# Kernel optimization log

Hardware: AMD Instinct MI355X
Metric: run time of the kernel (lower is better)

Reference implementation:

```python
import jax, jax.numpy as jnp
import numpy as np

B, E = 256, 512
C, K = 8192, 10          # n_class, n_center
LMD = 10.0
INV_GAMMA = 10.0         # 1 / gamma, gamma = 0.1
TAU = 0.2
MARGIN = 0.01


def setup_inputs() -> dict:
    key = jax.random.key(0)
    k1, k2, k3 = jax.random.split(key, 3)
    embeddings = jax.random.normal(k1, (B, E), dtype=jnp.float32)
    labels = jax.random.randint(k2, (B,), 0, C, dtype=jnp.int64)
    fc = jax.random.normal(k3, (C * K, E), dtype=jnp.float32)
    return {"embeddings": embeddings, "labels": labels, "fc": fc}


def reference(embeddings, labels, fc):
    # L2-normalize centers (rows of fc), like F.normalize(fc, p=2, dim=1)
    norm = jnp.sqrt(jnp.sum(fc * fc, axis=1, keepdims=True))
    w = fc / jnp.maximum(norm, 1e-12)

    # similarity to every center: [B, C, K]
    x = (embeddings @ w.T).reshape(B, C, K)
    prob = jax.nn.softmax(INV_GAMMA * x, axis=2)
    h = jnp.sum(prob * x, axis=2)  # [B, C] soft-pooled class similarity

    # subtract margin on ground-truth class, then cross-entropy
    rows = jnp.arange(B)
    margin_m = jnp.zeros_like(h).at[rows, labels].set(MARGIN)
    logits = LMD * (h - margin_m)
    logp = jax.nn.log_softmax(logits, axis=1)
    loss_cls = -jnp.mean(logp[rows, labels])

    # regularizer: batched per-class center gram, replaces python loop over C
    wc = w.reshape(C, K, E)
    sub = 1.0 - jnp.einsum('cke,cje->ckj', wc, wc)   # [C, K, K]
    sub = jnp.where(sub <= 0.0, 1e-10, sub)
    mask = jnp.triu(jnp.ones((K, K), dtype=bool), k=1)  # strict upper triangle
    safe = jnp.where(mask, 2.0 * sub, 1.0)
    reg = jnp.sum(jnp.where(mask, jnp.sqrt(safe), 0.0))
    reg = reg / (C * K * (K - 1.0))
    return loss_cls + TAU * reg
```

## Files before the change

### kernel.cpp

```cpp
#include <hip/hip_runtime.h>


typedef __bf16 bf16;
typedef bf16 bf16x8 __attribute__((ext_vector_type(8)));
typedef float f32x4 __attribute__((ext_vector_type(4)));

#define NCLASS 8192
#define KC 10
#define KPAD 16
#define EDIM 512
#define BATCH 256

__device__ inline void load_lds16(const void* g, void* l) {
    __builtin_amdgcn_global_load_lds(
        (const __attribute__((address_space(1))) void*)g,
        (__attribute__((address_space(3))) void*)l, 16, 0, 0);
}

__global__ __launch_bounds__(256) void prep_kernel(
    const float* __restrict__ fc, bf16* __restrict__ wpad,
    float* __restrict__ gram_part)
{
    __shared__ float rows[KC * EDIM];
    __shared__ float s_invn[KC];
    __shared__ float s_wsum[4];
    const int c = blockIdx.x;
    const int t = threadIdx.x;
    const int wave = t >> 6, lane = t & 63;

    const float4* src = (const float4*)(fc + (size_t)c * (KC * EDIM));
    float4* rows4 = (float4*)rows;
    #pragma unroll
    for (int i = 0; i < 5; ++i) rows4[t + i * 256] = src[t + i * 256];
    __syncthreads();

    for (int r = wave; r < KC; r += 4) {
        float s = 0.f;
        #pragma unroll
        for (int j = 0; j < 8; ++j) {
            float v = rows[r * EDIM + lane + j * 64];
            s += v * v;
        }
        #pragma unroll
        for (int off = 32; off; off >>= 1) s += __shfl_xor(s, off);
        if (lane == 0) s_invn[r] = 1.0f / fmaxf(sqrtf(s), 1e-12f);
    }
    __syncthreads();

    bf16x8* dst = (bf16x8*)(wpad + (size_t)c * (KPAD * EDIM));
    #pragma unroll
    for (int p = 0; p < 4; ++p) {
        int j = t + p * 256;
        int r = j >> 6;
        bf16x8 v;
        if (r < KC) {
            float inv = s_invn[r];
            float4 a = *(const float4*)(rows + j * 8);
            float4 b = *(const float4*)(rows + j * 8 + 4);
            v[0] = (bf16)(a.x * inv); v[1] = (bf16)(a.y * inv);
            v[2] = (bf16)(a.z * inv); v[3] = (bf16)(a.w * inv);
            v[4] = (bf16)(b.x * inv); v[5] = (bf16)(b.y * inv);
            v[6] = (bf16)(b.z * inv); v[7] = (bf16)(b.w * inv);
        } else {
            #pragma unroll
            for (int u = 0; u < 8; ++u) v[u] = (bf16)0.0f;
        }
        dst[j] = v;
    }

    float part = 0.f;
    for (int p = wave; p < 45; p += 4) {
        int i = 0, pp = p;
        while (pp >= 9 - i) { pp -= 9 - i; ++i; }
        int j = i + 1 + pp;
        float s = 0.f;
        #pragma unroll
        for (int u = 0; u < 8; ++u)
            s += rows[i * EDIM + lane + u * 64] * rows[j * EDIM + lane + u * 64];
        #pragma unroll
        for (int off = 32; off; off >>= 1) s += __shfl_xor(s, off);
        if (lane == 0) {
            float sub = 1.0f - s * s_invn[i] * s_invn[j];
            if (sub <= 0.0f) sub = 1e-10f;
            part += sqrtf(2.0f * sub);
        }
    }
    if (lane == 0) s_wsum[wave] = part;
    __syncthreads();
    if (t == 0) gram_part[c] = s_wsum[0] + s_wsum[1] + s_wsum[2] + s_wsum[3];
}

__global__ __launch_bounds__(256) void conv_kernel(
    const float* __restrict__ e, bf16* __restrict__ out)
{
    int i = blockIdx.x * 256 + threadIdx.x;
    float4 a = ((const float4*)e)[i * 2];
    float4 b = ((const float4*)e)[i * 2 + 1];
    bf16x8 v;
    v[0] = (bf16)a.x; v[1] = (bf16)a.y; v[2] = (bf16)a.z; v[3] = (bf16)a.w;
    v[4] = (bf16)b.x; v[5] = (bf16)b.y; v[6] = (bf16)b.z; v[7] = (bf16)b.w;
    ((bf16x8*)out)[i] = v;
}

__global__ __launch_bounds__(512) void gemm_h_kernel(
    const bf16* __restrict__ W,
    const bf16* __restrict__ A,
    float* __restrict__ h)
{
    __shared__ bf16 Ws[128 * 32];
    __shared__ bf16 Es[256 * 32];
    const int tid = threadIdx.x;
    const int wave = tid >> 6, lane = tid & 63;
    const int wm = wave & 1, wn = wave >> 1;
    const size_t m0 = (size_t)blockIdx.x * 128;

    f32x4 acc[4][4];
    #pragma unroll
    for (int mt = 0; mt < 4; ++mt)
        #pragma unroll
        for (int nt = 0; nt < 4; ++nt)
            acc[mt][nt] = (f32x4){0.f, 0.f, 0.f, 0.f};

    const int lrow = lane >> 2;
    const int lcol = (lane & 3) * 8;

    for (int kb = 0; kb < EDIM; kb += 32) {
        load_lds16(W + (m0 + wave * 16 + lrow) * EDIM + kb + lcol,
                   Ws + (wave * 16) * 32);
        #pragma unroll
        for (int p = 0; p < 2; ++p) {
            int row = p * 128 + wave * 16 + lrow;
            load_lds16(A + row * EDIM + kb + lcol,
                       Es + (p * 128 + wave * 16) * 32);
        }
        __syncthreads();

        const int q8 = (lane >> 4) * 8;
        bf16x8 wf[4], ef[4];
        #pragma unroll
        for (int mt = 0; mt < 4; ++mt)
            wf[mt] = *(const bf16x8*)&Ws[(wm * 64 + mt * 16 + (lane & 15)) * 32 + q8];
        #pragma unroll
        for (int nt = 0; nt < 4; ++nt)
            ef[nt] = *(const bf16x8*)&Es[(wn * 64 + nt * 16 + (lane & 15)) * 32 + q8];
        #pragma unroll
        for (int mt = 0; mt < 4; ++mt)
            #pragma unroll
            for (int nt = 0; nt < 4; ++nt)
                acc[mt][nt] = __builtin_amdgcn_mfma_f32_16x16x32_bf16(
                    wf[mt], ef[nt], acc[mt][nt], 0, 0, 0);
        __syncthreads();
    }

    const int col = lane & 15;
    const int quad = lane >> 4;
    #pragma unroll
    for (int mt = 0; mt < 4; ++mt) {
        int cls = blockIdx.x * 8 + wm * 4 + mt;
        #pragma unroll
        for (int nt = 0; nt < 4; ++nt) {
            int b = wn * 64 + nt * 16 + col;
            float xm = -1e30f;
            #pragma unroll
            for (int r = 0; r < 4; ++r)
                if (quad * 4 + r < KC) xm = fmaxf(xm, acc[mt][nt][r]);
            xm = fmaxf(xm, __shfl_xor(xm, 16));
            xm = fmaxf(xm, __shfl_xor(xm, 32));
            float s1 = 0.f, s2 = 0.f;
            #pragma unroll
            for (int r = 0; r < 4; ++r) {
                if (quad * 4 + r < KC) {
                    float x = acc[mt][nt][r];
                    float e = __expf(10.0f * (x - xm));
                    s1 += e; s2 += e * x;
                }
            }
            s1 += __shfl_xor(s1, 16); s1 += __shfl_xor(s1, 32);
            s2 += __shfl_xor(s2, 16); s2 += __shfl_xor(s2, 32);
            if (quad == 0) h[(size_t)b * NCLASS + cls] = s2 / s1;
        }
    }
}

__global__ __launch_bounds__(256) void ce_kernel(
    const float* __restrict__ h, const int* __restrict__ labels,
    float* __restrict__ ce_part)
{
    __shared__ float redm[4];
    __shared__ float reds[4];
    const int b = blockIdx.x, t = threadIdx.x;
    const int wave = t >> 6, lane = t & 63;
    const int lbl = labels[b];
    const float* hb = h + (size_t)b * NCLASS;

    float lg_cache[32];
    float mx = -1e30f;
    #pragma unroll
    for (int k = 0; k < 32; ++k) {
        int c = t + k * 256;
        float lg = 10.0f * hb[c];
        if (c == lbl) lg -= 0.1f;
        lg_cache[k] = lg;
        mx = fmaxf(mx, lg);
    }
    #pragma unroll
    for (int off = 32; off; off >>= 1) mx = fmaxf(mx, __shfl_xor(mx, off));
    if (lane == 0) redm[wave] = mx;
    __syncthreads();
    mx = fmaxf(fmaxf(redm[0], redm[1]), fmaxf(redm[2], redm[3]));

    float s = 0.f;
    #pragma unroll
    for (int k = 0; k < 32; ++k) s += __expf(lg_cache[k] - mx);
    #pragma unroll
    for (int off = 32; off; off >>= 1) s += __shfl_xor(s, off);
    if (lane == 0) reds[wave] = s;
    __syncthreads();
    if (t == 0) {
        s = reds[0] + reds[1] + reds[2] + reds[3];
        float logit_l = 10.0f * (hb[lbl] - 0.01f);
        ce_part[b] = mx + logf(s) - logit_l;
    }
}

__global__ __launch_bounds__(256) void final_kernel(
    const float* __restrict__ gram_part, const float* __restrict__ ce_part,
    float* __restrict__ out)
{
    __shared__ float red[4];
    const int t = threadIdx.x, wave = t >> 6, lane = t & 63;
    float g = 0.f;
    #pragma unroll
    for (int i = 0; i < 32; ++i) g += gram_part[t + i * 256];
    float val = ce_part[t] * (1.0f / 256.0f)
              + g * (0.2f / 737280.0f);
    #pragma unroll
    for (int off = 32; off; off >>= 1) val += __shfl_xor(val, off);
    if (lane == 0) red[wave] = val;
    __syncthreads();
    if (t == 0) out[0] = red[0] + red[1] + red[2] + red[3];
}

extern "C" void kernel_launch(void* const* d_in, const int* in_sizes, int n_in,
                              void* d_out, int out_size, void* d_ws, size_t ws_size,
                              hipStream_t stream) {
    const float* emb    = (const float*)d_in[0];
    const int*   labels = (const int*)d_in[1];
    const float* fc     = (const float*)d_in[2];
    float* out = (float*)d_out;

    char* ws = (char*)d_ws;
    bf16*  wpad      = (bf16*)ws;
    bf16*  embb      = (bf16*)(ws + 134217728);
    float* h         = (float*)(ws + 134479872);
    float* gram_part = (float*)(ws + 142868480);
    float* ce_part   = (float*)(ws + 142901248);

    prep_kernel<<<NCLASS, 256, 0, stream>>>(fc, wpad, gram_part);
    conv_kernel<<<64, 256, 0, stream>>>(emb, embb);
    gemm_h_kernel<<<131072 / 128, 512, 0, stream>>>(wpad, embb, h);
    ce_kernel<<<BATCH, 256, 0, stream>>>(h, labels, ce_part);
    final_kernel<<<1, 256, 0, stream>>>(gram_part, ce_part, out);
}
```

Measured before the change: 326.6 us.

## Store unnormalized bf16 centers unpadded, apply norms in GEMM epilogue, split CE

The prep kernel now writes raw bf16 centers with no padding from 10 to 16 rows, plus a per-class inverse-norm table, and computes norms and the gram regularizer from the bf16 copy. The GEMM drops LDS staging and barriers, loads fragments straight from global memory, and scales by inverse norms before the soft-pool epilogue. h is written transposed, and cross-entropy becomes a class-split online softmax that a final kernel merges. This aims to cut weight write and read traffic and to spread the CE work over more blocks, at the cost of uncoalesced direct global fragment loads and computing the regularizer from bf16 values.

```diff
diff --git a/kernel.cpp b/kernel.cpp
--- a/kernel.cpp
+++ b/kernel.cpp
@@ -3,91 +3,83 @@
 
 typedef __bf16 bf16;
 typedef bf16 bf16x8 __attribute__((ext_vector_type(8)));
+typedef bf16 bf16x4 __attribute__((ext_vector_type(4)));
+typedef bf16 bf16x2 __attribute__((ext_vector_type(2)));
 typedef float f32x4 __attribute__((ext_vector_type(4)));
 
 #define NCLASS 8192
 #define KC 10
-#define KPAD 16
 #define EDIM 512
 #define BATCH 256
 
-__device__ inline void load_lds16(const void* g, void* l) {
-    __builtin_amdgcn_global_load_lds(
-        (const __attribute__((address_space(1))) void*)g,
-        (__attribute__((address_space(3))) void*)l, 16, 0, 0);
-}
-
-__global__ __launch_bounds__(256) void prep_kernel(
-    const float* __restrict__ fc, bf16* __restrict__ wpad,
-    float* __restrict__ gram_part)
-{
-    __shared__ float rows[KC * EDIM];
+__global__ __launch_bounds__(320) void prep_kernel(
+    const float* __restrict__ fc, bf16* __restrict__ w,
+    float* __restrict__ invn, float* __restrict__ gram_part)
+{
+    __shared__ bf16 rb[KC * EDIM];
     __shared__ float s_invn[KC];
-    __shared__ float s_wsum[4];
-    const int c = blockIdx.x;
-    const int t = threadIdx.x;
+    __shared__ float s_part[5];
+    const int c = blockIdx.x, t = threadIdx.x;
     const int wave = t >> 6, lane = t & 63;
 
     const float4* src = (const float4*)(fc + (size_t)c * (KC * EDIM));
-    float4* rows4 = (float4*)rows;
-    #pragma unroll
-    for (int i = 0; i < 5; ++i) rows4[t + i * 256] = src[t + i * 256];
-    __syncthreads();
-
-    for (int r = wave; r < KC; r += 4) {
+    bf16x4* wdst = (bf16x4*)(w + (size_t)c * (KC * EDIM));
+    bf16x4* ldst = (bf16x4*)rb;
+    #pragma unroll
+    for (int p = 0; p < 4; ++p) {
+        int idx = t + p * 320;
+        float4 v = src[idx];
+        bf16x4 bv;
+        bv[0] = (bf16)v.x; bv[1] = (bf16)v.y;
+        bv[2] = (bf16)v.z; bv[3] = (bf16)v.w;
+        ldst[idx] = bv;
+        wdst[idx] = bv;
+    }
+    __syncthreads();
+
+    #pragma unroll
+    for (int rr = 0; rr < 2; ++rr) {
+        int r = wave * 2 + rr;
         float s = 0.f;
         #pragma unroll
-        for (int j = 0; j < 8; ++j) {
-            float v = rows[r * EDIM + lane + j * 64];
-            s += v * v;
+        for (int j = 0; j < 4; ++j) {
+            bf16x2 v = *(const bf16x2*)&rb[r * EDIM + (lane + j * 64) * 2];
+            float a = (float)v[0], b = (float)v[1];
+            s += a * a + b * b;
         }
         #pragma unroll
         for (int off = 32; off; off >>= 1) s += __shfl_xor(s, off);
         if (lane == 0) s_invn[r] = 1.0f / fmaxf(sqrtf(s), 1e-12f);
     }
     __syncthreads();
-
-    bf16x8* dst = (bf16x8*)(wpad + (size_t)c * (KPAD * EDIM));
-    #pragma unroll
-    for (int p = 0; p < 4; ++p) {
-        int j = t + p * 256;
-        int r = j >> 6;
-        bf16x8 v;
-        if (r < KC) {
-            float inv = s_invn[r];
-            float4 a = *(const float4*)(rows + j * 8);
-            float4 b = *(const float4*)(rows + j * 8 + 4);
-            v[0] = (bf16)(a.x * inv); v[1] = (bf16)(a.y * inv);
-            v[2] = (bf16)(a.z * inv); v[3] = (bf16)(a.w * inv);
-            v[4] = (bf16)(b.x * inv); v[5] = (bf16)(b.y * inv);
-            v[6] = (bf16)(b.z * inv); v[7] = (bf16)(b.w * inv);
-        } else {
-            #pragma unroll
-            for (int u = 0; u < 8; ++u) v[u] = (bf16)0.0f;
-        }
-        dst[j] = v;
-    }
+    if (t < 16) invn[(size_t)c * 16 + t] = (t < KC) ? s_invn[t] : 0.0f;
 
     float part = 0.f;
-    for (int p = wave; p < 45; p += 4) {
+    #pragma unroll
+    for (int q = 0; q < 9; ++q) {
+        int p = wave * 9 + q;
         int i = 0, pp = p;
         while (pp >= 9 - i) { pp -= 9 - i; ++i; }
         int j = i + 1 + pp;
         float s = 0.f;
         #pragma unroll
-        for (int u = 0; u < 8; ++u)
-            s += rows[i * EDIM + lane + u * 64] * rows[j * EDIM + lane + u * 64];
+        for (int u = 0; u < 4; ++u) {
+            bf16x2 a = *(const bf16x2*)&rb[i * EDIM + (lane + u * 64) * 2];
+            bf16x2 b = *(const bf16x2*)&rb[j * EDIM + (lane + u * 64) * 2];
+            s += (float)a[0] * (float)b[0] + (float)a[1] * (float)b[1];
+        }
         #pragma unroll
         for (int off = 32; off; off >>= 1) s += __shfl_xor(s, off);
         if (lane == 0) {
             float sub = 1.0f - s * s_invn[i] * s_invn[j];
-            if (sub <= 0.0f) sub = 1e-10f;
+            if (sub <= 0.f) sub = 1e-10f;
             part += sqrtf(2.0f * sub);
         }
     }
-    if (lane == 0) s_wsum[wave] = part;
-    __syncthreads();
-    if (t == 0) gram_part[c] = s_wsum[0] + s_wsum[1] + s_wsum[2] + s_wsum[3];
+    if (lane == 0) s_part[wave] = part;
+    __syncthreads();
+    if (t == 0)
+        gram_part[c] = s_part[0] + s_part[1] + s_part[2] + s_part[3] + s_part[4];
 }
 
 __global__ __launch_bounds__(256) void conv_kernel(
@@ -102,17 +94,24 @@
     ((bf16x8*)out)[i] = v;
 }
 
-__global__ __launch_bounds__(512) void gemm_h_kernel(
-    const bf16* __restrict__ W,
-    const bf16* __restrict__ A,
-    float* __restrict__ h)
-{
-    __shared__ bf16 Ws[128 * 32];
-    __shared__ bf16 Es[256 * 32];
+__global__ __launch_bounds__(256) void gemm_h_kernel(
+    const bf16* __restrict__ w, const bf16* __restrict__ embb,
+    const float* __restrict__ invn, float* __restrict__ hT)
+{
     const int tid = threadIdx.x;
     const int wave = tid >> 6, lane = tid & 63;
-    const int wm = wave & 1, wn = wave >> 1;
-    const size_t m0 = (size_t)blockIdx.x * 128;
+    const int m16 = lane & 15, quad = lane >> 4;
+    const int cgrp = blockIdx.x;
+    const int clamp_m = (m16 < KC) ? m16 : 0;
+
+    const bf16* wp[4];
+    const bf16* ep[4];
+    #pragma unroll
+    for (int mt = 0; mt < 4; ++mt)
+        wp[mt] = w + ((size_t)(cgrp * 4 + mt) * KC + clamp_m) * EDIM + quad * 8;
+    #pragma unroll
+    for (int nt = 0; nt < 4; ++nt)
+        ep[nt] = embb + (size_t)(wave * 64 + nt * 16 + m16) * EDIM + quad * 8;
 
     f32x4 acc[4][4];
     #pragma unroll
@@ -121,119 +120,93 @@
         for (int nt = 0; nt < 4; ++nt)
             acc[mt][nt] = (f32x4){0.f, 0.f, 0.f, 0.f};
 
-    const int lrow = lane >> 2;
-    const int lcol = (lane & 3) * 8;
-
+    #pragma unroll
     for (int kb = 0; kb < EDIM; kb += 32) {
-        load_lds16(W + (m0 + wave * 16 + lrow) * EDIM + kb + lcol,
-                   Ws + (wave * 16) * 32);
-        #pragma unroll
-        for (int p = 0; p < 2; ++p) {
-            int row = p * 128 + wave * 16 + lrow;
-            load_lds16(A + row * EDIM + kb + lcol,
-                       Es + (p * 128 + wave * 16) * 32);
-        }
-        __syncthreads();
-
-        const int q8 = (lane >> 4) * 8;
         bf16x8 wf[4], ef[4];
         #pragma unroll
         for (int mt = 0; mt < 4; ++mt)
-            wf[mt] = *(const bf16x8*)&Ws[(wm * 64 + mt * 16 + (lane & 15)) * 32 + q8];
+            wf[mt] = *(const bf16x8*)(wp[mt] + kb);
         #pragma unroll
         for (int nt = 0; nt < 4; ++nt)
-            ef[nt] = *(const bf16x8*)&Es[(wn * 64 + nt * 16 + (lane & 15)) * 32 + q8];
+            ef[nt] = *(const bf16x8*)(ep[nt] + kb);
         #pragma unroll
         for (int mt = 0; mt < 4; ++mt)
             #pragma unroll
             for (int nt = 0; nt < 4; ++nt)
                 acc[mt][nt] = __builtin_amdgcn_mfma_f32_16x16x32_bf16(
                     wf[mt], ef[nt], acc[mt][nt], 0, 0, 0);
-        __syncthreads();
-    }
-
-    const int col = lane & 15;
-    const int quad = lane >> 4;
+    }
+
     #pragma unroll
     for (int mt = 0; mt < 4; ++mt) {
-        int cls = blockIdx.x * 8 + wm * 4 + mt;
+        int cls = cgrp * 4 + mt;
+        float4 iv = *(const float4*)(invn + (size_t)cls * 16 + quad * 4);
         #pragma unroll
         for (int nt = 0; nt < 4; ++nt) {
-            int b = wn * 64 + nt * 16 + col;
+            float x[4];
             float xm = -1e30f;
             #pragma unroll
-            for (int r = 0; r < 4; ++r)
-                if (quad * 4 + r < KC) xm = fmaxf(xm, acc[mt][nt][r]);
+            for (int r = 0; r < 4; ++r) {
+                x[r] = acc[mt][nt][r] * ((const float*)&iv)[r];
+                if (quad * 4 + r < KC) xm = fmaxf(xm, x[r]);
+            }
             xm = fmaxf(xm, __shfl_xor(xm, 16));
             xm = fmaxf(xm, __shfl_xor(xm, 32));
             float s1 = 0.f, s2 = 0.f;
             #pragma unroll
             for (int r = 0; r < 4; ++r) {
                 if (quad * 4 + r < KC) {
-                    float x = acc[mt][nt][r];
-                    float e = __expf(10.0f * (x - xm));
-                    s1 += e; s2 += e * x;
+                    float e = __expf(10.0f * (x[r] - xm));
+                    s1 += e; s2 += e * x[r];
                 }
             }
             s1 += __shfl_xor(s1, 16); s1 += __shfl_xor(s1, 32);
             s2 += __shfl_xor(s2, 16); s2 += __shfl_xor(s2, 32);
-            if (quad == 0) h[(size_t)b * NCLASS + cls] = s2 / s1;
+            if (quad == 0)
+                hT[(size_t)cls * BATCH + wave * 64 + nt * 16 + m16] = s2 / s1;
         }
     }
 }
 
 __global__ __launch_bounds__(256) void ce_kernel(
-    const float* __restrict__ h, const int* __restrict__ labels,
-    float* __restrict__ ce_part)
-{
-    __shared__ float redm[4];
-    __shared__ float reds[4];
-    const int b = blockIdx.x, t = threadIdx.x;
-    const int wave = t >> 6, lane = t & 63;
+    const float* __restrict__ hT, const int* __restrict__ labels,
+    float* __restrict__ part_m, float* __restrict__ part_s)
+{
+    const int s = blockIdx.x, b = threadIdx.x;
     const int lbl = labels[b];
-    const float* hb = h + (size_t)b * NCLASS;
-
-    float lg_cache[32];
-    float mx = -1e30f;
-    #pragma unroll
-    for (int k = 0; k < 32; ++k) {
-        int c = t + k * 256;
-        float lg = 10.0f * hb[c];
-        if (c == lbl) lg -= 0.1f;
-        lg_cache[k] = lg;
-        mx = fmaxf(mx, lg);
-    }
-    #pragma unroll
-    for (int off = 32; off; off >>= 1) mx = fmaxf(mx, __shfl_xor(mx, off));
-    if (lane == 0) redm[wave] = mx;
-    __syncthreads();
-    mx = fmaxf(fmaxf(redm[0], redm[1]), fmaxf(redm[2], redm[3]));
-
-    float s = 0.f;
-    #pragma unroll
-    for (int k = 0; k < 32; ++k) s += __expf(lg_cache[k] - mx);
-    #pragma unroll
-    for (int off = 32; off; off >>= 1) s += __shfl_xor(s, off);
-    if (lane == 0) reds[wave] = s;
-    __syncthreads();
-    if (t == 0) {
-        s = reds[0] + reds[1] + reds[2] + reds[3];
-        float logit_l = 10.0f * (hb[lbl] - 0.01f);
-        ce_part[b] = mx + logf(s) - logit_l;
-    }
+    const int c0 = s * 128;
+    float m = -1e30f, sum = 0.f;
+    for (int i = 0; i < 128; ++i) {
+        int c = c0 + i;
+        float x = 10.0f * hT[(size_t)c * BATCH + b];
+        if (c == lbl) x -= 0.1f;
+        if (x > m) { sum = sum * __expf(m - x) + 1.0f; m = x; }
+        else sum += __expf(x - m);
+    }
+    part_m[s * BATCH + b] = m;
+    part_s[s * BATCH + b] = sum;
 }
 
 __global__ __launch_bounds__(256) void final_kernel(
-    const float* __restrict__ gram_part, const float* __restrict__ ce_part,
-    float* __restrict__ out)
+    const float* __restrict__ part_m, const float* __restrict__ part_s,
+    const float* __restrict__ hT, const int* __restrict__ labels,
+    const float* __restrict__ gram_part, float* __restrict__ out)
 {
     __shared__ float red[4];
     const int t = threadIdx.x, wave = t >> 6, lane = t & 63;
+    float M = -1e30f, S = 0.f;
+    for (int s = 0; s < 64; ++s) {
+        float m = part_m[s * BATCH + t], ss = part_s[s * BATCH + t];
+        if (m > M) { S = S * __expf(M - m) + ss; M = m; }
+        else S += ss * __expf(m - M);
+    }
+    int lbl = labels[t];
+    float xl = 10.0f * hT[(size_t)lbl * BATCH + t] - 0.1f;
+    float ce = M + logf(S) - xl;
     float g = 0.f;
     #pragma unroll
     for (int i = 0; i < 32; ++i) g += gram_part[t + i * 256];
-    float val = ce_part[t] * (1.0f / 256.0f)
-              + g * (0.2f / 737280.0f);
+    float val = ce * (1.0f / 256.0f) + g * (0.2f / 737280.0f);
     #pragma unroll
     for (int off = 32; off; off >>= 1) val += __shfl_xor(val, off);
     if (lane == 0) red[wave] = val;
@@ -250,15 +223,17 @@
     float* out = (float*)d_out;
 
     char* ws = (char*)d_ws;
-    bf16*  wpad      = (bf16*)ws;
-    bf16*  embb      = (bf16*)(ws + 134217728);
-    float* h         = (float*)(ws + 134479872);
-    float* gram_part = (float*)(ws + 142868480);
-    float* ce_part   = (float*)(ws + 142901248);
-
-    prep_kernel<<<NCLASS, 256, 0, stream>>>(fc, wpad, gram_part);
+    bf16*  w         = (bf16*)ws;
+    bf16*  embb      = (bf16*)(ws + 83886080);
+    float* hT        = (float*)(ws + 84148224);
+    float* invn      = (float*)(ws + 92536832);
+    float* gram_part = (float*)(ws + 93061120);
+    float* part_m    = (float*)(ws + 93093888);
+    float* part_s    = (float*)(ws + 93159424);
+
+    prep_kernel<<<NCLASS, 320, 0, stream>>>(fc, w, invn, gram_part);
     conv_kernel<<<64, 256, 0, stream>>>(emb, embb);
-    gemm_h_kernel<<<131072 / 128, 512, 0, stream>>>(wpad, embb, h);
-    ce_kernel<<<BATCH, 256, 0, stream>>>(h, labels, ce_part);
-    final_kernel<<<1, 256, 0, stream>>>(gram_part, ce_part, out);
-}
+    gemm_h_kernel<<<2048, 256, 0, stream>>>(w, embb, invn, hT);
+    ce_kernel<<<64, 256, 0, stream>>>(hT, labels, part_m, part_s);
+    final_kernel<<<1, 256, 0, stream>>>(part_m, part_s, hT, labels, gram_part, out);
+}
```

Result: slower. 419.3 us (+28.4%).
